# Kernel tuning notes

Measured on AMD Instinct MI355X. Metric: run time of the kernel, lower is better.

## Reference

```python
import jax, jax.numpy as jnp
import numpy as np

# ---- config (mirrors init_kwargs) ----
D_MODEL = 1024
D_STATE = 128
EXPAND = 2
HEADDIM = 64
D_INNER = D_MODEL * EXPAND            # 2048
NHEADS = D_INNER // HEADDIM           # 32
ROPE_FRACTION = 0.5
ROTATE_DIM = (int(D_STATE * ROPE_FRACTION) // 2) * 2   # 64
NUM_ANGLES = ROTATE_DIM // 2          # 32
A_FLOOR = 1e-4
EPS = 1e-5
IN_PROJ_DIM = 2 * D_INNER + 2 * D_STATE + 3 * NHEADS + NUM_ANGLES  # 4480
BATCH, SEQLEN = 2, 2048


def _state_rmsnorm(x, w):
    rms = jnp.sqrt(jnp.mean(x * x, axis=-1, keepdims=True) + EPS)
    return x / rms * w


def _apply_rotary_pairs(x, phase):
    # x: (b,s,h,d_state), phase: (b,s,h,num_pairs)
    if ROTATE_DIM == 0:
        return x
    x_rot = x[..., :ROTATE_DIM].reshape(*x.shape[:-1], ROTATE_DIM // 2, 2)
    x_pass = x[..., ROTATE_DIM:]
    cos = jnp.cos(phase)
    sin = jnp.sin(phase)
    real = x_rot[..., 0]
    imag = x_rot[..., 1]
    rr = real * cos - imag * sin
    ri = real * sin + imag * cos
    rotated = jnp.stack([rr, ri], axis=-1).reshape(*x.shape[:-1], ROTATE_DIM)
    if x_pass.shape[-1] == 0:
        return rotated
    return jnp.concatenate([rotated, x_pass], axis=-1)


def setup_inputs() -> dict:
    key = jax.random.key(0)
    ks = jax.random.split(key, 5)
    x = jax.random.normal(ks[0], (BATCH, SEQLEN, D_MODEL), jnp.float32)
    W_in = jax.random.normal(ks[1], (IN_PROJ_DIM, D_MODEL), jnp.float32) / np.sqrt(D_MODEL)
    # dt_bias ~ inverse-softplus of dt sampled in [dt_min, dt_max]
    dt = jnp.exp(jax.random.uniform(ks[2], (NHEADS,), jnp.float32) * (np.log(0.1) - np.log(0.001)) + np.log(0.001))
    dt = jnp.clip(dt, 1e-4)
    dt_bias = dt + jnp.log(-jnp.expm1(-dt))
    B_norm_w = jnp.ones((D_STATE,), jnp.float32)
    C_norm_w = jnp.ones((D_STATE,), jnp.float32)
    B_bias = jnp.ones((NHEADS, D_STATE), jnp.float32)
    C_bias = jnp.ones((NHEADS, D_STATE), jnp.float32)
    D_param = jnp.ones((NHEADS,), jnp.float32)
    out_norm_w = jnp.ones((D_INNER,), jnp.float32)
    W_out = jax.random.normal(ks[3], (D_MODEL, D_INNER), jnp.float32) / np.sqrt(D_INNER)
    return {"x": x, "W_in": W_in, "dt_bias": dt_bias, "B_norm_w": B_norm_w,
            "C_norm_w": C_norm_w, "B_bias": B_bias, "C_bias": C_bias,
            "D_param": D_param, "out_norm_w": out_norm_w, "W_out": W_out}


def reference(x, W_in, dt_bias, B_norm_w, C_norm_w, B_bias, C_bias, D_param, out_norm_w, W_out):
    b, s, _ = x.shape
    proj = jnp.einsum('bsd,pd->bsp', x, W_in)
    sizes = [D_INNER, D_INNER, D_STATE, D_STATE, NHEADS, NHEADS, NHEADS, NUM_ANGLES]
    offs = np.cumsum([0] + sizes)
    z, v, B_raw, C_raw, dd_dt, dd_A, trap_logits, angle_logits = [
        proj[..., offs[i]:offs[i + 1]] for i in range(8)]
    z = z.reshape(b, s, NHEADS, HEADDIM)
    v = v.reshape(b, s, NHEADS, HEADDIM)
    Bm = _state_rmsnorm(B_raw, B_norm_w)[:, :, None, :] + B_bias[None, None]   # (b,s,h,n)
    Cm = _state_rmsnorm(C_raw, C_norm_w)[:, :, None, :] + C_bias[None, None]
    dt = jax.nn.softplus(dd_dt + dt_bias[None, None])          # (b,s,h)
    A = jnp.minimum(-jax.nn.softplus(dd_A), -A_FLOOR)          # (b,s,h)
    trap = jax.nn.sigmoid(trap_logits)                          # (b,s,h)
    phase = jnp.cumsum(angle_logits, axis=1)[:, :, None, :]     # (b,s,1,angles)
    phase = jnp.broadcast_to(phase, (b, s, NHEADS, NUM_ANGLES))
    Bm = _apply_rotary_pairs(Bm, phase)
    Cm = _apply_rotary_pairs(Cm, phase)

    alpha = jnp.exp(A * dt)               # (b,s,h)
    beta = (1.0 - trap) * dt * alpha
    gamma = trap * dt

    # move time to leading for scan: (s, b, h, ...)
    def tl(a):
        return jnp.moveaxis(a, 1, 0)
    xs = (tl(alpha), tl(beta), tl(gamma), tl(Bm), tl(Cm), tl(v))

    state0 = jnp.zeros((b, NHEADS, HEADDIM, D_STATE), jnp.float32)
    pk0 = jnp.zeros((b, NHEADS, D_STATE), jnp.float32)
    pv0 = jnp.zeros((b, NHEADS, HEADDIM), jnp.float32)

    def step(carry, inp):
        state, pk, pv = carry
        a_t, b_t, g_t, k_t, q_t, v_t = inp
        prev_outer = pv[..., :, None] * pk[..., None, :]        # (b,h,p,n)
        curr_outer = v_t[..., :, None] * k_t[..., None, :]
        state = (a_t[..., None, None] * state
                 + b_t[..., None, None] * prev_outer
                 + g_t[..., None, None] * curr_outer)
        y_t = jnp.einsum('bhpn,bhn->bhp', state, q_t) + D_param[None, :, None] * v_t
        return (state, k_t, v_t), y_t

    _, ys = jax.lax.scan(step, (state0, pk0, pv0), xs)
    y = jnp.moveaxis(ys, 0, 1).reshape(b, s, D_INNER)
    z = z.reshape(b, s, D_INNER)
    # GatedRMSNorm
    rms = jnp.sqrt(jnp.mean(y * y, axis=-1, keepdims=True) + EPS)
    y = (y / rms * out_norm_w) * jax.nn.silu(z)
    return jnp.einsum('bsi,di->bsd', y, W_out)
```

## Files before the change

### kernel.cpp

```cpp
#include <hip/hip_runtime.h>
#include <math.h>

#define S_LEN 2048
#define NBATCH 2
#define DMODEL 1024
#define PDIM 4480
#define DI 2048
#define NH 32
#define HD 64
#define DS 128
#define NA 32
#define CHK 64
#define NC (S_LEN / CHK)
#define ZV 4096
#define PS 384
#define PS_B 0
#define PS_C 128
#define PS_DT 256
#define PS_A 288
#define PS_TRAP 320
#define PS_ANG 352

typedef __attribute__((ext_vector_type(8))) short s8v;
typedef __attribute__((ext_vector_type(4))) float f4v;

__device__ __forceinline__ float softplus_f(float x) {
    return x > 20.f ? x : log1pf(expf(x));
}

__device__ __forceinline__ ushort f2bf(float f) {
    unsigned u = __float_as_uint(f);
    unsigned r = (u + 0x7fffu + ((u >> 16) & 1u)) >> 16;
    return (ushort)r;
}

__device__ __forceinline__ uint4 pack8(const float* f) {
    uint4 o;
    o.x = (unsigned)f2bf(f[0]) | ((unsigned)f2bf(f[1]) << 16);
    o.y = (unsigned)f2bf(f[2]) | ((unsigned)f2bf(f[3]) << 16);
    o.z = (unsigned)f2bf(f[4]) | ((unsigned)f2bf(f[5]) << 16);
    o.w = (unsigned)f2bf(f[6]) | ((unsigned)f2bf(f[7]) << 16);
    return o;
}

__device__ __forceinline__ float bf2f(ushort u) {
    return __uint_as_float(((unsigned)u) << 16);
}
__device__ __forceinline__ float bf_lo(unsigned u) { return __uint_as_float(u << 16); }
__device__ __forceinline__ float bf_hi(unsigned u) { return __uint_as_float(u & 0xffff0000u); }

__device__ __forceinline__ void unpack8(uint4 a, float* f) {
    f[0] = bf_lo(a.x); f[1] = bf_hi(a.x);
    f[2] = bf_lo(a.y); f[3] = bf_hi(a.y);
    f[4] = bf_lo(a.z); f[5] = bf_hi(a.z);
    f[6] = bf_lo(a.w); f[7] = bf_hi(a.w);
}

#define NCX  524288
#define NCWI 573440
#define NCWO 262144
__global__ __launch_bounds__(256)
void f2bf_all(const float* __restrict__ x, const float* __restrict__ wi,
              const float* __restrict__ wo, ushort* __restrict__ xbf,
              ushort* __restrict__ wibf, ushort* __restrict__ wobf) {
    int idx = blockIdx.x * 256 + threadIdx.x;
    const float* src; ushort* dst; int shift, rel;
    if (idx < NCX)              { rel = idx;               src = x;  dst = xbf;  shift = 7; }
    else if (idx < NCX + NCWI)  { rel = idx - NCX;         src = wi; dst = wibf; shift = 7; }
    else                        { rel = idx - NCX - NCWI;  src = wo; dst = wobf; shift = 8; }
    int dc = rel ^ ((rel >> shift) & 7);
    const float* ip = src + (size_t)rel * 8;
    float4 v0 = *(const float4*)ip;
    float4 v1 = *(const float4*)(ip + 4);
    uint4 o;
    o.x = (unsigned)f2bf(v0.x) | ((unsigned)f2bf(v0.y) << 16);
    o.y = (unsigned)f2bf(v0.z) | ((unsigned)f2bf(v0.w) << 16);
    o.z = (unsigned)f2bf(v1.x) | ((unsigned)f2bf(v1.y) << 16);
    o.w = (unsigned)f2bf(v1.z) | ((unsigned)f2bf(v1.w) << 16);
    *(uint4*)(dst + (size_t)dc * 8) = o;
}

__global__ __launch_bounds__(256, 2)
void gemm_bf16(const ushort* __restrict__ A, const ushort* __restrict__ B,
               float* __restrict__ Cf, ushort* __restrict__ Cb,
               int M, int N, int K, int split, int fstride, int SW) {
    __shared__ __align__(16) short lAB[2][128 * 64];
    short* lA = &lAB[0][0];
    short* lB = &lAB[1][0];
    int nwg = gridDim.x;
    int bid = blockIdx.x;
    int chunk = nwg >> 3;
    int swz = (bid & 7) * chunk + (bid >> 3);
    int nb = N >> 7;
    int sup = 4 * SW;
    int st = swz / sup, w = swz % sup;
    int stPerRow = nb / SW;
    int by = (st / stPerRow) * 4 + w / SW;
    int bx = (st % stPerRow) * SW + w % SW;

    int tid = threadIdx.x;
    int wv = tid >> 6, ln = tid & 63;
    int rl = ln & 15, kg = ln >> 4, r7 = rl & 7;
    int R0 = (wv >> 1) * 64, C0 = (wv & 1) * 64;

    const ushort* Ag = A + (size_t)(by * 128 + wv * 32 + (ln >> 3)) * K + (ln & 7) * 8;
    const ushort* Bg = B + (size_t)(bx * 128 + wv * 32 + (ln >> 3)) * K + (ln & 7) * 8;
    short* lAw = lA + (wv * 32) * 64;
    short* lBw = lB + (wv * 32) * 64;

    f4v acc[4][4];
#pragma unroll
    for (int m = 0; m < 4; ++m)
#pragma unroll
        for (int n = 0; n < 4; ++n) acc[m][n] = f4v{0.f, 0.f, 0.f, 0.f};

    for (int k0 = 0; k0 < K; k0 += 64) {
        __syncthreads();
#pragma unroll
        for (int i = 0; i < 4; ++i) {
            __builtin_amdgcn_global_load_lds(
                (const __attribute__((address_space(1))) void*)(Ag + (size_t)i * 8 * K + k0),
                (__attribute__((address_space(3))) void*)(lAw + i * 8 * 64), 16, 0, 0);
            __builtin_amdgcn_global_load_lds(
                (const __attribute__((address_space(1))) void*)(Bg + (size_t)i * 8 * K + k0),
                (__attribute__((address_space(3))) void*)(lBw + i * 8 * 64), 16, 0, 0);
        }
        __syncthreads();
#pragma unroll
        for (int ks = 0; ks < 2; ++ks) {
            int kc = ks * 4 + kg;
            int co = ((kc ^ r7) << 3);
            s8v av[4], bv[4];
#pragma unroll
            for (int m = 0; m < 4; ++m)
                av[m] = *(const s8v*)&lA[(R0 + m * 16 + rl) * 64 + co];
#pragma unroll
            for (int n = 0; n < 4; ++n)
                bv[n] = *(const s8v*)&lB[(C0 + n * 16 + rl) * 64 + co];
#pragma unroll
            for (int m = 0; m < 4; ++m)
#pragma unroll
                for (int n = 0; n < 4; ++n)
                    acc[m][n] = __builtin_amdgcn_mfma_f32_16x16x32_bf16(
                        av[m], bv[n], acc[m][n], 0, 0, 0);
        }
    }
    if (bx * 128 < split) {
        __syncthreads();
        ushort* ct = (ushort*)lAB;
#pragma unroll
        for (int m = 0; m < 4; ++m)
#pragma unroll
            for (int n = 0; n < 4; ++n)
#pragma unroll
                for (int r = 0; r < 4; ++r)
                    ct[(R0 + m * 16 + kg * 4 + r) * 128 + C0 + n * 16 + rl] =
                        f2bf(acc[m][n][r]);
        __syncthreads();
        ushort* cb = Cb + (size_t)(by * 128) * split + bx * 128;
        const uint4* cs = (const uint4*)ct;
#pragma unroll
        for (int k = 0; k < 8; ++k) {
            int idx = k * 256 + tid;
            int row = idx >> 4, cc = idx & 15;
            *(uint4*)(cb + (size_t)row * split + cc * 8) = cs[idx];
        }
    } else {
#pragma unroll
        for (int hp = 0; hp < 2; ++hp) {
            __syncthreads();
            float* cf = (float*)lAB;
            if ((wv & 1) == hp) {
#pragma unroll
                for (int m = 0; m < 4; ++m)
#pragma unroll
                    for (int n = 0; n < 4; ++n)
#pragma unroll
                        for (int r = 0; r < 4; ++r)
                            cf[(R0 + m * 16 + kg * 4 + r) * 64 + n * 16 + rl] =
                                acc[m][n][r];
            }
            __syncthreads();
            float* co = Cf + (size_t)(by * 128) * fstride + (bx * 128 - split) + hp * 64;
            const float4* fs = (const float4*)cf;
#pragma unroll
            for (int k = 0; k < 8; ++k) {
                int idx = k * 256 + tid;
                int row = idx >> 4, c4 = idx & 15;
                *(float4*)(co + (size_t)row * fstride + c4 * 4) = fs[idx];
            }
        }
    }
}

__global__ __launch_bounds__(256)
void phase_kernel(const float* __restrict__ projS, float* __restrict__ cosb,
                  float* __restrict__ sinb) {
    int b = blockIdx.x >> 5;
    int j = blockIdx.x & 31;
    int tid = threadIdx.x;
    __shared__ float part[256];
    float v[8];
    float run = 0.f;
#pragma unroll
    for (int e = 0; e < 8; ++e) {
        int s = tid * 8 + e;
        v[e] = projS[((size_t)(b * S_LEN + s)) * PS + PS_ANG + j];
        run += v[e];
    }
    part[tid] = run;
    __syncthreads();
    for (int off = 1; off < 256; off <<= 1) {
        float add = (tid >= off) ? part[tid - off] : 0.f;
        __syncthreads();
        part[tid] += add;
        __syncthreads();
    }
    float acc = (tid > 0) ? part[tid - 1] : 0.f;
#pragma unroll
    for (int e = 0; e < 8; ++e) {
        acc += v[e];
        int s = tid * 8 + e;
        size_t o = ((size_t)(b * S_LEN + s)) * NA + j;
        cosb[o] = cosf(acc);
        sinb[o] = sinf(acc);
    }
}

__global__ __launch_bounds__(128)
void prep_kernel(const float* __restrict__ projS, const float* __restrict__ dt_bias,
                 const float* __restrict__ Bw, const float* __restrict__ Cw,
                 const float* __restrict__ cosb, const float* __restrict__ sinb,
                 float* __restrict__ Bn, float* __restrict__ Cn,
                 float* __restrict__ ldb, float* __restrict__ wbuf,
                 float* __restrict__ pubuf) {
    size_t row = blockIdx.x;
    int b = (int)(row >> 11);
    int s = (int)(row & 2047);
    int n = threadIdx.x;
    const float* pr = projS + row * PS;
    float vB = pr[PS_B + n];
    float vC = pr[PS_C + n];
    float sB = vB * vB, sC = vC * vC;
#pragma unroll
    for (int off = 32; off >= 1; off >>= 1) {
        sB += __shfl_xor(sB, off);
        sC += __shfl_xor(sC, off);
    }
    __shared__ float redB[2], redC[2];
    if ((n & 63) == 0) { redB[n >> 6] = sB; redC[n >> 6] = sC; }
    __syncthreads();
    float rB = sqrtf((redB[0] + redB[1]) * (1.f / 128.f) + 1e-5f);
    float rC = sqrtf((redC[0] + redC[1]) * (1.f / 128.f) + 1e-5f);
    float bn = vB / rB * Bw[n];
    float cn = vC / rC * Cw[n];
    float bp = __shfl_xor(bn, 1);
    float cp = __shfl_xor(cn, 1);
    float ob = bn, oc = cn;
    if (n < 64) {
        float c = cosb[row * NA + (n >> 1)];
        float sn_ = sinb[row * NA + (n >> 1)];
        if ((n & 1) == 0) { ob = bn * c - bp * sn_; oc = cn * c - cp * sn_; }
        else              { ob = bp * sn_ + bn * c; oc = cp * sn_ + cn * c; }
    }
    Bn[row * DS + n] = ob;
    Cn[row * DS + n] = oc;
    if (n < NH) {
        int h = n;
        float dtv = softplus_f(pr[PS_DT + h] + dt_bias[h]);
        float Av = -fmaxf(softplus_f(pr[PS_A + h]), 1e-4f);
        float trap = 1.f / (1.f + expf(-pr[PS_TRAP + h]));
        size_t o = ((size_t)(b * NH + h)) * S_LEN + s;
        ldb[o]   = Av * dtv;
        wbuf[o]  = trap * dtv;
        pubuf[o] = (1.f - trap) * dtv;
    }
}

__global__ __launch_bounds__(256)
void lcum_kernel(float* __restrict__ ell) {
    size_t row = blockIdx.x;
    int tid = threadIdx.x;
    float* p = ell + row * S_LEN;
    float v[8];
    float run = 0.f;
#pragma unroll
    for (int e = 0; e < 8; ++e) { v[e] = p[tid * 8 + e]; run += v[e]; }
    __shared__ float part[256];
    part[tid] = run;
    __syncthreads();
    for (int off = 1; off < 256; off <<= 1) {
        float add = (tid >= off) ? part[tid - off] : 0.f;
        __syncthreads();
        part[tid] += add;
        __syncthreads();
    }
    float acc = (tid > 0) ? part[tid - 1] : 0.f;
#pragma unroll
    for (int e = 0; e < 8; ++e) { acc += v[e]; p[tid * 8 + e] = acc; }
}

__device__ __forceinline__ void build32v(
    float* vals, const float* __restrict__ br, const float* __restrict__ bias,
    const float* __restrict__ cr, const float* __restrict__ sr, int rot) {
    float bv[32], bi[32];
#pragma unroll
    for (int j = 0; j < 8; ++j) *(float4*)&bv[j * 4] = *(const float4*)(br + j * 4);
#pragma unroll
    for (int j = 0; j < 8; ++j) *(float4*)&bi[j * 4] = *(const float4*)(bias + j * 4);
    if (rot) {
        float cf[16], sf[16];
#pragma unroll
        for (int j = 0; j < 4; ++j) {
            *(float4*)&cf[j * 4] = *(const float4*)(cr + j * 4);
            *(float4*)&sf[j * 4] = *(const float4*)(sr + j * 4);
        }
#pragma unroll
        for (int a = 0; a < 16; ++a) {
            float c = cf[a], s = sf[a], e = bi[2 * a], o = bi[2 * a + 1];
            vals[2 * a]     = bv[2 * a]     + e * c - o * s;
            vals[2 * a + 1] = bv[2 * a + 1] + e * s + o * c;
        }
    } else {
#pragma unroll
        for (int j = 0; j < 32; ++j) vals[j] = bv[j] + bi[j];
    }
}

__global__ __launch_bounds__(256, 4)
void delta_kernel(const ushort* __restrict__ zvbf, const float* __restrict__ Bn,
                  const float* __restrict__ cosb, const float* __restrict__ sinb,
                  const float* __restrict__ ell, const float* __restrict__ wbuf,
                  const float* __restrict__ pubuf, const float* __restrict__ B_bias,
                  ushort* __restrict__ dstate, ushort* __restrict__ vtbuf,
                  ushort* __restrict__ kbuf, float* __restrict__ rbuf) {
    __shared__ __align__(16) ushort KT[DS * CHK];
    __shared__ __align__(16) ushort cVT[HD * CHK];
    __shared__ __align__(16) ushort VT[HD * CHK];
    int blk = blockIdx.x;
    int c = blk & (NC - 1);
    int h = (blk >> 5) & (NH - 1);
    int b = blk >> 10;
    int tid = threadIdx.x;
    size_t row0 = (size_t)b * S_LEN + c * CHK;
    size_t bh = (size_t)b * NH + h;
    int i = tid >> 2, q4 = tid & 3;

    size_t so = bh * S_LEN + c * CHK + i;
    float llast = ell[bh * S_LEN + c * CHK + CHK - 1];
    float li = ell[so];
    float u = wbuf[so];
    if (c * CHK + i < S_LEN - 1) u += pubuf[so + 1];
    float coef = expf(llast - li) * u;
    if (tid == 0) {
        float base = (c == 0) ? 0.f : ell[bh * S_LEN + c * CHK - 1];
        rbuf[blk] = expf(llast - base);
    }
    {
        int n0 = q4 * 32;
        float vals[32];
        build32v(vals, Bn + (row0 + i) * DS + n0, B_bias + h * DS + n0,
                 cosb + (row0 + i) * NA + q4 * 16, sinb + (row0 + i) * NA + q4 * 16,
                 q4 < 2);
#pragma unroll
        for (int j = 0; j < 32; ++j) {
            int n = n0 + j;
            KT[n * 64 + (((i >> 3) ^ (n & 7)) << 3) + (i & 7)] = f2bf(vals[j]);
        }
        ushort* kd = kbuf + (size_t)blk * (CHK * DS);
#pragma unroll
        for (int j = 0; j < 4; ++j) {
            int cc = (q4 * 4 + j) ^ (i & 7);
            *(uint4*)&kd[i * 128 + cc * 8] = pack8(&vals[j * 8]);
        }
    }
    {
        int p0 = q4 * 16;
        const ushort* vp = zvbf + (size_t)(row0 + i) * ZV + 2048 + h * HD + p0;
        uint4 a0 = *(const uint4*)vp;
        uint4 a1 = *(const uint4*)(vp + 8);
        unsigned uu[8] = {a0.x, a0.y, a0.z, a0.w, a1.x, a1.y, a1.z, a1.w};
#pragma unroll
        for (int j = 0; j < 8; ++j) {
            ushort v0 = (ushort)(uu[j] & 0xffffu);
            ushort v1 = (ushort)(uu[j] >> 16);
            int p = p0 + 2 * j;
            int addr0 = p * 64 + (((i >> 3) ^ (p & 7)) << 3) + (i & 7);
            int addr1 = (p + 1) * 64 + (((i >> 3) ^ ((p + 1) & 7)) << 3) + (i & 7);
            VT[addr0]  = v0;
            VT[addr1]  = v1;
            cVT[addr0] = f2bf(bf2f(v0) * coef);
            cVT[addr1] = f2bf(bf2f(v1) * coef);
        }
    }
    __syncthreads();
    {
        const uint4* vs = (const uint4*)VT;
        uint4* vd = (uint4*)(vtbuf + (size_t)blk * (HD * CHK));
        vd[tid] = vs[tid];
        vd[tid + 256] = vs[tid + 256];
    }
    int wv = tid >> 6, ln = tid & 63, rl = ln & 15, kg = ln >> 4;
    int pA = wv * 16 + rl;
    s8v aV[2];
#pragma unroll
    for (int ks = 0; ks < 2; ++ks)
        aV[ks] = *(const s8v*)&cVT[pA * 64 + (((ks * 4 + kg) ^ (pA & 7)) << 3)];
    f4v dacc[8];
    __builtin_amdgcn_s_setprio(1);
#pragma unroll
    for (int nt = 0; nt < 8; ++nt) {
        int nB = nt * 16 + rl;
        dacc[nt] = f4v{0.f, 0.f, 0.f, 0.f};
#pragma unroll
        for (int ks = 0; ks < 2; ++ks) {
            s8v bK = *(const s8v*)&KT[nB * 64 + (((ks * 4 + kg) ^ (nB & 7)) << 3)];
            dacc[nt] = __builtin_amdgcn_mfma_f32_16x16x32_bf16(aV[ks], bK, dacc[nt], 0, 0, 0);
        }
    }
    __builtin_amdgcn_s_setprio(0);
    __syncthreads();
#pragma unroll
    for (int nt = 0; nt < 8; ++nt) {
#pragma unroll
        for (int r = 0; r < 4; ++r) {
            int p = wv * 16 + kg * 4 + r;
            int n = nt * 16 + rl;
            KT[p * 128 + (((n >> 3) ^ (p & 7)) << 3) + (n & 7)] = f2bf(dacc[nt][r]);
        }
    }
    __syncthreads();
    {
        const uint4* dsr = (const uint4*)KT;
        uint4* dd = (uint4*)(dstate + (size_t)blk * (HD * DS));
#pragma unroll
        for (int k = 0; k < 4; ++k) dd[k * 256 + tid] = dsr[k * 256 + tid];
    }
}

__global__ __launch_bounds__(256)
void state_prop(ushort* __restrict__ dstate, const float* __restrict__ rbuf) {
    int g = blockIdx.x;
    size_t bh = (size_t)(g >> 2);
    int sl = g & 3;
    int tid = threadIdx.x;
    float st[8];
#pragma unroll
    for (int j = 0; j < 8; ++j) st[j] = 0.f;
    uint4* base = (uint4*)dstate;
    size_t off0 = bh * NC * 1024ull + (size_t)sl * 256 + tid;
    uint4 nxt = base[off0];
    for (int c = 0; c < NC; ++c) {
        uint4 cur = nxt;
        if (c + 1 < NC) nxt = base[off0 + (size_t)(c + 1) * 1024];
        float r = rbuf[bh * NC + c];
        unsigned uu[4] = {cur.x, cur.y, cur.z, cur.w};
        unsigned oo[4];
#pragma unroll
        for (int e = 0; e < 4; ++e) {
            float d0 = bf_lo(uu[e]), d1 = bf_hi(uu[e]);
            int ix = e * 2;
            oo[e] = (unsigned)f2bf(st[ix]) | ((unsigned)f2bf(st[ix + 1]) << 16);
            st[ix]     = fmaf(r, st[ix], d0);
            st[ix + 1] = fmaf(r, st[ix + 1], d1);
        }
        base[off0 + (size_t)c * 1024] = uint4{oo[0], oo[1], oo[2], oo[3]};
    }
}

__global__ __launch_bounds__(256, 4)
void out_kernel(const float* __restrict__ Cn, const float* __restrict__ cosb,
                const float* __restrict__ sinb, const float* __restrict__ ell,
                const float* __restrict__ wbuf, const float* __restrict__ pubuf,
                const float* __restrict__ C_bias, const ushort* __restrict__ dstate,
                const ushort* __restrict__ vtbuf, const ushort* __restrict__ kbuf,
                float* __restrict__ yb) {
    __shared__ __align__(16) ushort Qb[CHK * DS];
    __shared__ __align__(16) ushort Kb[CHK * DS];
    __shared__ __align__(16) ushort VTb[HD * CHK];
    int blk = blockIdx.x;
    int c = blk & (NC - 1);
    int h = (blk >> 5) & (NH - 1);
    int b = blk >> 10;
    int tid = threadIdx.x;
    size_t row0 = (size_t)b * S_LEN + c * CHK;
    size_t bh = (size_t)b * NH + h;
    int i = tid >> 2, q4 = tid & 3;
    int wv2 = tid >> 6, ln = tid & 63;

    {
        const ushort* kg_ = kbuf + (size_t)blk * (CHK * DS);
#pragma unroll
        for (int k = 0; k < 4; ++k) {
            int ch = wv2 * 256 + k * 64;
            __builtin_amdgcn_global_load_lds(
                (const __attribute__((address_space(1))) void*)(kg_ + (size_t)(ch + ln) * 8),
                (__attribute__((address_space(3))) void*)(Kb + ch * 8), 16, 0, 0);
        }
        const ushort* vg = vtbuf + (size_t)blk * (HD * CHK);
#pragma unroll
        for (int k = 0; k < 2; ++k) {
            int ch = wv2 * 128 + k * 64;
            __builtin_amdgcn_global_load_lds(
                (const __attribute__((address_space(1))) void*)(vg + (size_t)(ch + ln) * 8),
                (__attribute__((address_space(3))) void*)(VTb + ch * 8), 16, 0, 0);
        }
    }
    {
        int n0 = q4 * 32;
        float vals[32];
        build32v(vals, Cn + (row0 + i) * DS + n0, C_bias + h * DS + n0,
                 cosb + (row0 + i) * NA + q4 * 16, sinb + (row0 + i) * NA + q4 * 16,
                 q4 < 2);
#pragma unroll
        for (int j = 0; j < 4; ++j) {
            int cc = (q4 * 4 + j) ^ (i & 7);
            *(uint4*)&Qb[i * 128 + cc * 8] = pack8(&vals[j * 8]);
        }
    }
    __syncthreads();

    int rl = ln & 15, kg = ln >> 4;
    int tA = wv2 * 16 + rl;
    s8v aQ[4];
#pragma unroll
    for (int kc = 0; kc < 4; ++kc)
        aQ[kc] = *(const s8v*)&Qb[tA * 128 + (((kc * 4 + kg) ^ (tA & 7)) << 3)];
    f4v pacc[4];
#pragma unroll
    for (int st = 0; st < 4; ++st) pacc[st] = f4v{0.f, 0.f, 0.f, 0.f};
    __builtin_amdgcn_s_setprio(1);
#pragma unroll
    for (int st = 0; st < 4; ++st) {
        int sB = st * 16 + rl;
#pragma unroll
        for (int kc = 0; kc < 4; ++kc) {
            s8v bK = *(const s8v*)&Kb[sB * 128 + (((kc * 4 + kg) ^ (sB & 7)) << 3)];
            pacc[st] = __builtin_amdgcn_mfma_f32_16x16x32_bf16(aQ[kc], bK, pacc[st], 0, 0, 0);
        }
    }
    __builtin_amdgcn_s_setprio(0);
    __syncthreads();

    {
        const ushort* sg = dstate + (size_t)blk * (CHK * DS);
#pragma unroll
        for (int k = 0; k < 4; ++k) {
            int ch = wv2 * 256 + k * 64;
            __builtin_amdgcn_global_load_lds(
                (const __attribute__((address_space(1))) void*)(sg + (size_t)(ch + ln) * 8),
                (__attribute__((address_space(3))) void*)(Kb + ch * 8), 16, 0, 0);
        }
    }
    size_t so0 = bh * S_LEN + c * CHK;
    float basev = (c == 0) ? 0.f : ell[so0 - 1];
    int t2r0 = wv2 * 16 + kg * 4;
    float et[4], wr[4];
#pragma unroll
    for (int r = 0; r < 4; ++r) {
        size_t so = so0 + t2r0 + r;
        et[r] = expf(ell[so] - basev);
        wr[r] = wbuf[so];
    }
    float fs[4];
#pragma unroll
    for (int st = 0; st < 4; ++st) {
        int s = st * 16 + rl;
        size_t sos = so0 + s;
        float u = wbuf[sos];
        if (c * CHK + s < S_LEN - 1) u += pubuf[sos + 1];
        fs[st] = u * expf(fminf(basev - ell[sos], 80.f));
    }
    ushort* PTb = Qb;
#pragma unroll
    for (int st = 0; st < 4; ++st) {
        int s = st * 16 + rl;
#pragma unroll
        for (int r = 0; r < 4; ++r) {
            int t2 = t2r0 + r;
            float m;
            if (s < t2)       m = et[r] * fs[st];
            else if (s == t2) m = wr[r];
            else              m = 0.f;
            PTb[t2 * 64 + (((s >> 3) ^ (t2 & 7)) << 3) + (s & 7)] = f2bf(pacc[st][r] * m);
        }
    }
    __syncthreads();

    s8v aP[2];
#pragma unroll
    for (int ks = 0; ks < 2; ++ks)
        aP[ks] = *(const s8v*)&PTb[tA * 64 + (((ks * 4 + kg) ^ (tA & 7)) << 3)];
    f4v y1[4], y2[4];
#pragma unroll
    for (int pt = 0; pt < 4; ++pt) { y1[pt] = f4v{0.f,0.f,0.f,0.f}; y2[pt] = f4v{0.f,0.f,0.f,0.f}; }
    __builtin_amdgcn_s_setprio(1);
#pragma unroll
    for (int pt = 0; pt < 4; ++pt) {
        int pB = pt * 16 + rl;
#pragma unroll
        for (int ks = 0; ks < 2; ++ks) {
            s8v bV = *(const s8v*)&VTb[pB * 64 + (((ks * 4 + kg) ^ (pB & 7)) << 3)];
            y1[pt] = __builtin_amdgcn_mfma_f32_16x16x32_bf16(aP[ks], bV, y1[pt], 0, 0, 0);
        }
#pragma unroll
        for (int kc = 0; kc < 4; ++kc) {
            s8v bS = *(const s8v*)&Kb[pB * 128 + (((kc * 4 + kg) ^ (pB & 7)) << 3)];
            y2[pt] = __builtin_amdgcn_mfma_f32_16x16x32_bf16(aQ[kc], bS, y2[pt], 0, 0, 0);
        }
    }
    __builtin_amdgcn_s_setprio(0);
    __syncthreads();
    float* ct = (float*)Qb;
#pragma unroll
    for (int pt = 0; pt < 4; ++pt) {
#pragma unroll
        for (int r = 0; r < 4; ++r) {
            int t2 = t2r0 + r;
            int p = pt * 16 + rl;
            ct[t2 * 64 + p] = y1[pt][r] + et[r] * y2[pt][r];
        }
    }
    __syncthreads();
    {
        float* yp = yb + (size_t)blk * (CHK * HD);
        const float4* fsrc = (const float4*)ct;
#pragma unroll
        for (int k = 0; k < 4; ++k) {
            int idx = k * 256 + tid;
            *(float4*)(yp + idx * 4) = fsrc[idx];
        }
    }
}

__global__ __launch_bounds__(256)
void ynorm_kernel(const float* __restrict__ yb, const ushort* __restrict__ zvbf,
                  const float* __restrict__ w, const float* __restrict__ D_param,
                  ushort* __restrict__ ybf) {
    size_t row = blockIdx.x;
    int b = (int)(row >> 11);
    int s = (int)(row & 2047);
    int c = s >> 6, t = s & 63;
    int tid = threadIdx.x;
    int hh = tid >> 3;
    int p0 = (tid * 8) & 63;
    const float* yr = yb + (((size_t)(b * NH + hh) * NC + c) * CHK + t) * HD + p0;
    float4 v0 = *(const float4*)yr;
    float4 v1 = *(const float4*)(yr + 4);
    float vvf[8];
    unpack8(*(const uint4*)(zvbf + row * (size_t)ZV + 2048 + tid * 8), vvf);
    float Dp = D_param[hh];
    float yv[8] = {v0.x + Dp * vvf[0], v0.y + Dp * vvf[1], v0.z + Dp * vvf[2], v0.w + Dp * vvf[3],
                   v1.x + Dp * vvf[4], v1.y + Dp * vvf[5], v1.z + Dp * vvf[6], v1.w + Dp * vvf[7]};
    float ss = 0.f;
#pragma unroll
    for (int e = 0; e < 8; ++e) ss += yv[e] * yv[e];
#pragma unroll
    for (int off = 32; off >= 1; off >>= 1) ss += __shfl_xor(ss, off);
    __shared__ float red[4];
    if ((tid & 63) == 0) red[tid >> 6] = ss;
    __syncthreads();
    float tot = red[0] + red[1] + red[2] + red[3];
    float rinv = 1.f / sqrtf(tot * (1.f / 2048.f) + 1e-5f);
    float zv[8];
    unpack8(*(const uint4*)(zvbf + row * (size_t)ZV + tid * 8), zv);
    float4 w0 = *(const float4*)(w + tid * 8);
    float4 w1 = *(const float4*)(w + tid * 8 + 4);
    float wv[8] = {w0.x, w0.y, w0.z, w0.w, w1.x, w1.y, w1.z, w1.w};
    ushort u[8];
#pragma unroll
    for (int e = 0; e < 8; ++e) {
        float sil = zv[e] / (1.f + expf(-zv[e]));
        u[e] = f2bf(yv[e] * rinv * wv[e] * sil);
    }
    int dstc = (tid & ~7) | ((tid & 7) ^ ((int)row & 7));
    uint4 o;
    o.x = (unsigned)u[0] | ((unsigned)u[1] << 16);
    o.y = (unsigned)u[2] | ((unsigned)u[3] << 16);
    o.z = (unsigned)u[4] | ((unsigned)u[5] << 16);
    o.w = (unsigned)u[6] | ((unsigned)u[7] << 16);
    *(uint4*)(ybf + row * (size_t)DI + dstc * 8) = o;
}

extern "C" void kernel_launch(void* const* d_in, const int* in_sizes, int n_in,
                              void* d_out, int out_size, void* d_ws, size_t ws_size,
                              hipStream_t stream) {
    const float* x          = (const float*)d_in[0];
    const float* W_in       = (const float*)d_in[1];
    const float* dt_bias    = (const float*)d_in[2];
    const float* B_norm_w   = (const float*)d_in[3];
    const float* C_norm_w   = (const float*)d_in[4];
    const float* B_bias     = (const float*)d_in[5];
    const float* C_bias     = (const float*)d_in[6];
    const float* D_param    = (const float*)d_in[7];
    const float* out_norm_w = (const float*)d_in[8];
    const float* W_out      = (const float*)d_in[9];
    float* out = (float*)d_out;

    const size_t M = (size_t)NBATCH * S_LEN;
    const size_t NBLK = (size_t)NBATCH * NH * NC;
    float* ws = (float*)d_ws;
    size_t off = 0;
    float* projS = ws + off; off += M * PS;
    float* cosb  = ws + off; off += M * NA;
    float* sinb  = ws + off; off += M * NA;
    float* Bn    = ws + off; off += M * DS;
    float* Cn    = ws + off; off += M * DS;
    float* ell   = ws + off; off += (size_t)NBATCH * NH * S_LEN;
    float* wbuf  = ws + off; off += (size_t)NBATCH * NH * S_LEN;
    float* pubuf = ws + off; off += (size_t)NBATCH * NH * S_LEN;
    float* yb    = ws + off; off += NBLK * CHK * HD;
    float* rbuf  = ws + off; off += NBLK;
    ushort* zvbf = (ushort*)(ws + off); off += M * ZV / 2;
    ushort* xbf  = (ushort*)(ws + off); off += M * DMODEL / 2;
    ushort* wibf = (ushort*)(ws + off); off += (size_t)PDIM * DMODEL / 2;
    ushort* wobf = (ushort*)(ws + off); off += (size_t)DMODEL * DI / 2;
    ushort* ybf  = (ushort*)(ws + off); off += M * DI / 2;
    ushort* dstate = (ushort*)(ws + off); off += NBLK * CHK * DS / 2;
    ushort* vtbuf  = (ushort*)(ws + off); off += NBLK * HD * CHK / 2;
    ushort* kbuf   = (ushort*)(ws + off); off += NBLK * CHK * DS / 2;

    f2bf_all<<<dim3((NCX + NCWI + NCWO) / 256), 256, 0, stream>>>(
        x, W_in, W_out, xbf, wibf, wobf);
    gemm_bf16<<<dim3((PDIM / 128) * (int)(M / 128)), 256, 0, stream>>>(
        xbf, wibf, projS, zvbf, (int)M, PDIM, DMODEL, ZV, PS, 5);
    phase_kernel<<<dim3(NBATCH * NA), 256, 0, stream>>>(projS, cosb, sinb);
    prep_kernel<<<dim3((int)M), 128, 0, stream>>>(projS, dt_bias, B_norm_w, C_norm_w,
                                                  cosb, sinb, Bn, Cn, ell, wbuf, pubuf);
    lcum_kernel<<<dim3(NBATCH * NH), 256, 0, stream>>>(ell);
    delta_kernel<<<dim3((int)NBLK), 256, 0, stream>>>(zvbf, Bn, cosb, sinb, ell,
                                                      wbuf, pubuf, B_bias, dstate,
                                                      vtbuf, kbuf, rbuf);
    state_prop<<<dim3(NBATCH * NH * 4), 256, 0, stream>>>(dstate, rbuf);
    out_kernel<<<dim3((int)NBLK), 256, 0, stream>>>(Cn, cosb, sinb, ell,
                                                    wbuf, pubuf, C_bias,
                                                    dstate, vtbuf, kbuf, yb);
    ynorm_kernel<<<dim3((int)M), 256, 0, stream>>>(yb, zvbf, out_norm_w, D_param, ybf);
    gemm_bf16<<<dim3((DMODEL / 128) * (int)(M / 128)), 256, 0, stream>>>(
        ybf, wobf, out, nullptr, (int)M, DMODEL, DI, 0, DMODEL, 4);
}
```

Measured before the change: 216.4 us.

## Move intra-chunk output into delta kernel; leave only inter-chunk term for post-scan

```diff
diff --git a/kernel.cpp b/kernel.cpp
--- a/kernel.cpp
+++ b/kernel.cpp
@@ -327,15 +327,17 @@
     }
 }
 
-__global__ __launch_bounds__(256, 4)
-void delta_kernel(const ushort* __restrict__ zvbf, const float* __restrict__ Bn,
-                  const float* __restrict__ cosb, const float* __restrict__ sinb,
-                  const float* __restrict__ ell, const float* __restrict__ wbuf,
-                  const float* __restrict__ pubuf, const float* __restrict__ B_bias,
-                  ushort* __restrict__ dstate, ushort* __restrict__ vtbuf,
-                  ushort* __restrict__ kbuf, float* __restrict__ rbuf) {
-    __shared__ __align__(16) ushort KT[DS * CHK];
-    __shared__ __align__(16) ushort cVT[HD * CHK];
+__global__ __launch_bounds__(256, 2)
+void intra_kernel(const ushort* __restrict__ zvbf, const float* __restrict__ Bn,
+                  const float* __restrict__ Cn, const float* __restrict__ cosb,
+                  const float* __restrict__ sinb, const float* __restrict__ ell,
+                  const float* __restrict__ wbuf, const float* __restrict__ pubuf,
+                  const float* __restrict__ B_bias, const float* __restrict__ C_bias,
+                  ushort* __restrict__ dstate, ushort* __restrict__ qbuf,
+                  float* __restrict__ yb, float* __restrict__ rbuf) {
+    __shared__ __align__(16) ushort cKT[DS * CHK];
+    __shared__ __align__(16) ushort bufK[CHK * DS];
+    __shared__ __align__(16) ushort bufQ[CHK * DS];
     __shared__ __align__(16) ushort VT[HD * CHK];
     int blk = blockIdx.x;
     int c = blk & (NC - 1);
@@ -363,15 +365,26 @@
                  cosb + (row0 + i) * NA + q4 * 16, sinb + (row0 + i) * NA + q4 * 16,
                  q4 < 2);
 #pragma unroll
+        for (int j = 0; j < 4; ++j) {
+            int cc = (q4 * 4 + j) ^ (i & 7);
+            *(uint4*)&bufK[i * 128 + cc * 8] = pack8(&vals[j * 8]);
+        }
+#pragma unroll
         for (int j = 0; j < 32; ++j) {
             int n = n0 + j;
-            KT[n * 64 + (((i >> 3) ^ (n & 7)) << 3) + (i & 7)] = f2bf(vals[j]);
-        }
-        ushort* kd = kbuf + (size_t)blk * (CHK * DS);
+            cKT[n * 64 + (((i >> 3) ^ (n & 7)) << 3) + (i & 7)] = f2bf(vals[j] * coef);
+        }
+    }
+    {
+        int n0 = q4 * 32;
+        float vals[32];
+        build32v(vals, Cn + (row0 + i) * DS + n0, C_bias + h * DS + n0,
+                 cosb + (row0 + i) * NA + q4 * 16, sinb + (row0 + i) * NA + q4 * 16,
+                 q4 < 2);
 #pragma unroll
         for (int j = 0; j < 4; ++j) {
             int cc = (q4 * 4 + j) ^ (i & 7);
-            *(uint4*)&kd[i * 128 + cc * 8] = pack8(&vals[j * 8]);
+            *(uint4*)&bufQ[i * 128 + cc * 8] = pack8(&vals[j * 8]);
         }
     }
     {
@@ -385,56 +398,143 @@
             ushort v0 = (ushort)(uu[j] & 0xffffu);
             ushort v1 = (ushort)(uu[j] >> 16);
             int p = p0 + 2 * j;
-            int addr0 = p * 64 + (((i >> 3) ^ (p & 7)) << 3) + (i & 7);
-            int addr1 = (p + 1) * 64 + (((i >> 3) ^ ((p + 1) & 7)) << 3) + (i & 7);
-            VT[addr0]  = v0;
-            VT[addr1]  = v1;
-            cVT[addr0] = f2bf(bf2f(v0) * coef);
-            cVT[addr1] = f2bf(bf2f(v1) * coef);
-        }
-    }
-    __syncthreads();
-    {
-        const uint4* vs = (const uint4*)VT;
-        uint4* vd = (uint4*)(vtbuf + (size_t)blk * (HD * CHK));
-        vd[tid] = vs[tid];
-        vd[tid + 256] = vs[tid + 256];
-    }
-    int wv = tid >> 6, ln = tid & 63, rl = ln & 15, kg = ln >> 4;
-    int pA = wv * 16 + rl;
+            VT[p * 64 + (((i >> 3) ^ (p & 7)) << 3) + (i & 7)] = v0;
+            VT[(p + 1) * 64 + (((i >> 3) ^ ((p + 1) & 7)) << 3) + (i & 7)] = v1;
+        }
+    }
+    __syncthreads();
+
+    int wv2 = tid >> 6, ln = tid & 63, rl = ln & 15, kg = ln >> 4;
+    int tA = wv2 * 16 + rl;
+    s8v aQ[4];
+#pragma unroll
+    for (int kc = 0; kc < 4; ++kc)
+        aQ[kc] = *(const s8v*)&bufQ[tA * 128 + (((kc * 4 + kg) ^ (tA & 7)) << 3)];
     s8v aV[2];
 #pragma unroll
     for (int ks = 0; ks < 2; ++ks)
-        aV[ks] = *(const s8v*)&cVT[pA * 64 + (((ks * 4 + kg) ^ (pA & 7)) << 3)];
+        aV[ks] = *(const s8v*)&VT[tA * 64 + (((ks * 4 + kg) ^ (tA & 7)) << 3)];
+    f4v pacc[4];
+#pragma unroll
+    for (int st = 0; st < 4; ++st) pacc[st] = f4v{0.f, 0.f, 0.f, 0.f};
     f4v dacc[8];
+#pragma unroll
+    for (int nt = 0; nt < 8; ++nt) dacc[nt] = f4v{0.f, 0.f, 0.f, 0.f};
     __builtin_amdgcn_s_setprio(1);
+#pragma unroll
+    for (int st = 0; st < 4; ++st) {
+        int sB = st * 16 + rl;
+#pragma unroll
+        for (int kc = 0; kc < 4; ++kc) {
+            s8v bK = *(const s8v*)&bufK[sB * 128 + (((kc * 4 + kg) ^ (sB & 7)) << 3)];
+            pacc[st] = __builtin_amdgcn_mfma_f32_16x16x32_bf16(aQ[kc], bK, pacc[st], 0, 0, 0);
+        }
+    }
 #pragma unroll
     for (int nt = 0; nt < 8; ++nt) {
         int nB = nt * 16 + rl;
-        dacc[nt] = f4v{0.f, 0.f, 0.f, 0.f};
 #pragma unroll
         for (int ks = 0; ks < 2; ++ks) {
-            s8v bK = *(const s8v*)&KT[nB * 64 + (((ks * 4 + kg) ^ (nB & 7)) << 3)];
+            s8v bK = *(const s8v*)&cKT[nB * 64 + (((ks * 4 + kg) ^ (nB & 7)) << 3)];
             dacc[nt] = __builtin_amdgcn_mfma_f32_16x16x32_bf16(aV[ks], bK, dacc[nt], 0, 0, 0);
         }
     }
     __builtin_amdgcn_s_setprio(0);
-    __syncthreads();
+    {
+        const uint4* qs = (const uint4*)bufQ;
+        uint4* qd = (uint4*)(qbuf + (size_t)blk * (CHK * DS));
+#pragma unroll
+        for (int k = 0; k < 4; ++k) qd[k * 256 + tid] = qs[k * 256 + tid];
+    }
+    __syncthreads();
+
+    size_t so0 = bh * S_LEN + c * CHK;
+    float basev = (c == 0) ? 0.f : ell[so0 - 1];
+    int t2r0 = wv2 * 16 + kg * 4;
+    float et[4], wr[4];
+#pragma unroll
+    for (int r = 0; r < 4; ++r) {
+        size_t sor = so0 + t2r0 + r;
+        et[r] = expf(ell[sor] - basev);
+        wr[r] = wbuf[sor];
+    }
+    float fs[4];
+#pragma unroll
+    for (int st = 0; st < 4; ++st) {
+        int s = st * 16 + rl;
+        size_t sos = so0 + s;
+        float uu = wbuf[sos];
+        if (c * CHK + s < S_LEN - 1) uu += pubuf[sos + 1];
+        fs[st] = uu * expf(fminf(basev - ell[sos], 80.f));
+    }
+    ushort* PTb = bufK;
+#pragma unroll
+    for (int st = 0; st < 4; ++st) {
+        int s = st * 16 + rl;
+#pragma unroll
+        for (int r = 0; r < 4; ++r) {
+            int t2 = t2r0 + r;
+            float m;
+            if (s < t2)       m = et[r] * fs[st];
+            else if (s == t2) m = wr[r];
+            else              m = 0.f;
+            PTb[t2 * 64 + (((s >> 3) ^ (t2 & 7)) << 3) + (s & 7)] = f2bf(pacc[st][r] * m);
+        }
+    }
 #pragma unroll
     for (int nt = 0; nt < 8; ++nt) {
 #pragma unroll
         for (int r = 0; r < 4; ++r) {
-            int p = wv * 16 + kg * 4 + r;
+            int p = wv2 * 16 + kg * 4 + r;
             int n = nt * 16 + rl;
-            KT[p * 128 + (((n >> 3) ^ (p & 7)) << 3) + (n & 7)] = f2bf(dacc[nt][r]);
-        }
-    }
-    __syncthreads();
+            cKT[p * 128 + (((n >> 3) ^ (p & 7)) << 3) + (n & 7)] = f2bf(dacc[nt][r]);
+        }
+    }
+    __syncthreads();
+
     {
-        const uint4* dsr = (const uint4*)KT;
+        const uint4* dsr = (const uint4*)cKT;
         uint4* dd = (uint4*)(dstate + (size_t)blk * (HD * DS));
 #pragma unroll
         for (int k = 0; k < 4; ++k) dd[k * 256 + tid] = dsr[k * 256 + tid];
+    }
+    s8v aP[2];
+#pragma unroll
+    for (int ks = 0; ks < 2; ++ks)
+        aP[ks] = *(const s8v*)&PTb[tA * 64 + (((ks * 4 + kg) ^ (tA & 7)) << 3)];
+    f4v y1[4];
+#pragma unroll
+    for (int pt = 0; pt < 4; ++pt) y1[pt] = f4v{0.f, 0.f, 0.f, 0.f};
+    __builtin_amdgcn_s_setprio(1);
+#pragma unroll
+    for (int pt = 0; pt < 4; ++pt) {
+        int pB = pt * 16 + rl;
+#pragma unroll
+        for (int ks = 0; ks < 2; ++ks) {
+            s8v bV = *(const s8v*)&VT[pB * 64 + (((ks * 4 + kg) ^ (pB & 7)) << 3)];
+            y1[pt] = __builtin_amdgcn_mfma_f32_16x16x32_bf16(aP[ks], bV, y1[pt], 0, 0, 0);
+        }
+    }
+    __builtin_amdgcn_s_setprio(0);
+    float* ct = (float*)bufQ;
+#pragma unroll
+    for (int pt = 0; pt < 4; ++pt) {
+#pragma unroll
+        for (int r = 0; r < 4; ++r) {
+            int t2 = t2r0 + r;
+            int p = pt * 16 + rl;
+            ct[t2 * 64 + p] = y1[pt][r];
+        }
+    }
+    __syncthreads();
+    {
+        float* yp = yb + (size_t)blk * (CHK * HD);
+        const float4* fsrc = (const float4*)ct;
+#pragma unroll
+        for (int k = 0; k < 4; ++k) {
+            int idx = k * 256 + tid;
+            *(float4*)(yp + idx * 4) = fsrc[idx];
+        }
     }
 }
 
@@ -469,144 +569,57 @@
 }
 
 __global__ __launch_bounds__(256, 4)
-void out_kernel(const float* __restrict__ Cn, const float* __restrict__ cosb,
-                const float* __restrict__ sinb, const float* __restrict__ ell,
-                const float* __restrict__ wbuf, const float* __restrict__ pubuf,
-                const float* __restrict__ C_bias, const ushort* __restrict__ dstate,
-                const ushort* __restrict__ vtbuf, const ushort* __restrict__ kbuf,
-                float* __restrict__ yb) {
+void y2_kernel(const ushort* __restrict__ qbuf, const ushort* __restrict__ dstate,
+               const float* __restrict__ ell, float* __restrict__ yb) {
     __shared__ __align__(16) ushort Qb[CHK * DS];
-    __shared__ __align__(16) ushort Kb[CHK * DS];
-    __shared__ __align__(16) ushort VTb[HD * CHK];
+    __shared__ __align__(16) ushort Sb[CHK * DS];
     int blk = blockIdx.x;
     int c = blk & (NC - 1);
     int h = (blk >> 5) & (NH - 1);
     int b = blk >> 10;
     int tid = threadIdx.x;
-    size_t row0 = (size_t)b * S_LEN + c * CHK;
     size_t bh = (size_t)b * NH + h;
-    int i = tid >> 2, q4 = tid & 3;
     int wv2 = tid >> 6, ln = tid & 63;
 
     {
-        const ushort* kg_ = kbuf + (size_t)blk * (CHK * DS);
+        const ushort* qg = qbuf + (size_t)blk * (CHK * DS);
+        const ushort* sg = dstate + (size_t)blk * (CHK * DS);
 #pragma unroll
         for (int k = 0; k < 4; ++k) {
             int ch = wv2 * 256 + k * 64;
             __builtin_amdgcn_global_load_lds(
-                (const __attribute__((address_space(1))) void*)(kg_ + (size_t)(ch + ln) * 8),
-                (__attribute__((address_space(3))) void*)(Kb + ch * 8), 16, 0, 0);
-        }
-        const ushort* vg = vtbuf + (size_t)blk * (HD * CHK);
-#pragma unroll
-        for (int k = 0; k < 2; ++k) {
-            int ch = wv2 * 128 + k * 64;
+                (const __attribute__((address_space(1))) void*)(qg + (size_t)(ch + ln) * 8),
+                (__attribute__((address_space(3))) void*)(Qb + ch * 8), 16, 0, 0);
             __builtin_amdgcn_global_load_lds(
-                (const __attribute__((address_space(1))) void*)(vg + (size_t)(ch + ln) * 8),
-                (__attribute__((address_space(3))) void*)(VTb + ch * 8), 16, 0, 0);
-        }
-    }
-    {
-        int n0 = q4 * 32;
-        float vals[32];
-        build32v(vals, Cn + (row0 + i) * DS + n0, C_bias + h * DS + n0,
-                 cosb + (row0 + i) * NA + q4 * 16, sinb + (row0 + i) * NA + q4 * 16,
-                 q4 < 2);
-#pragma unroll
-        for (int j = 0; j < 4; ++j) {
-            int cc = (q4 * 4 + j) ^ (i & 7);
-            *(uint4*)&Qb[i * 128 + cc * 8] = pack8(&vals[j * 8]);
-        }
-    }
-    __syncthreads();
-
+                (const __attribute__((address_space(1))) void*)(sg + (size_t)(ch + ln) * 8),
+                (__attribute__((address_space(3))) void*)(Sb + ch * 8), 16, 0, 0);
+        }
+    }
+    size_t so0 = bh * S_LEN + c * CHK;
+    float basev = (c == 0) ? 0.f : ell[so0 - 1];
     int rl = ln & 15, kg = ln >> 4;
+    int t2r0 = wv2 * 16 + kg * 4;
+    float et[4];
+#pragma unroll
+    for (int r = 0; r < 4; ++r) et[r] = expf(ell[so0 + t2r0 + r] - basev);
+    __syncthreads();
+
     int tA = wv2 * 16 + rl;
     s8v aQ[4];
 #pragma unroll
     for (int kc = 0; kc < 4; ++kc)
         aQ[kc] = *(const s8v*)&Qb[tA * 128 + (((kc * 4 + kg) ^ (tA & 7)) << 3)];
-    f4v pacc[4];
-#pragma unroll
-    for (int st = 0; st < 4; ++st) pacc[st] = f4v{0.f, 0.f, 0.f, 0.f};
-    __builtin_amdgcn_s_setprio(1);
-#pragma unroll
-    for (int st = 0; st < 4; ++st) {
-        int sB = st * 16 + rl;
-#pragma unroll
-        for (int kc = 0; kc < 4; ++kc) {
-            s8v bK = *(const s8v*)&Kb[sB * 128 + (((kc * 4 + kg) ^ (sB & 7)) << 3)];
-            pacc[st] = __builtin_amdgcn_mfma_f32_16x16x32_bf16(aQ[kc], bK, pacc[st], 0, 0, 0);
-        }
-    }
-    __builtin_amdgcn_s_setprio(0);
-    __syncthreads();
-
-    {
-        const ushort* sg = dstate + (size_t)blk * (CHK * DS);
-#pragma unroll
-        for (int k = 0; k < 4; ++k) {
-            int ch = wv2 * 256 + k * 64;
-            __builtin_amdgcn_global_load_lds(
-                (const __attribute__((address_space(1))) void*)(sg + (size_t)(ch + ln) * 8),
-                (__attribute__((address_space(3))) void*)(Kb + ch * 8), 16, 0, 0);
-        }
-    }
-    size_t so0 = bh * S_LEN + c * CHK;
-    float basev = (c == 0) ? 0.f : ell[so0 - 1];
-    int t2r0 = wv2 * 16 + kg * 4;
-    float et[4], wr[4];
-#pragma unroll
-    for (int r = 0; r < 4; ++r) {
-        size_t so = so0 + t2r0 + r;
-        et[r] = expf(ell[so] - basev);
-        wr[r] = wbuf[so];
-    }
-    float fs[4];
-#pragma unroll
-    for (int st = 0; st < 4; ++st) {
-        int s = st * 16 + rl;
-        size_t sos = so0 + s;
-        float u = wbuf[sos];
-        if (c * CHK + s < S_LEN - 1) u += pubuf[sos + 1];
-        fs[st] = u * expf(fminf(basev - ell[sos], 80.f));
-    }
-    ushort* PTb = Qb;
-#pragma unroll
-    for (int st = 0; st < 4; ++st) {
-        int s = st * 16 + rl;
-#pragma unroll
-        for (int r = 0; r < 4; ++r) {
-            int t2 = t2r0 + r;
-            float m;
-            if (s < t2)       m = et[r] * fs[st];
-            else if (s == t2) m = wr[r];
-            else              m = 0.f;
-            PTb[t2 * 64 + (((s >> 3) ^ (t2 & 7)) << 3) + (s & 7)] = f2bf(pacc[st][r] * m);
-        }
-    }
-    __syncthreads();
-
-    s8v aP[2];
-#pragma unroll
-    for (int ks = 0; ks < 2; ++ks)
-        aP[ks] = *(const s8v*)&PTb[tA * 64 + (((ks * 4 + kg) ^ (tA & 7)) << 3)];
-    f4v y1[4], y2[4];
-#pragma unroll
-    for (int pt = 0; pt < 4; ++pt) { y1[pt] = f4v{0.f,0.f,0.f,0.f}; y2[pt] = f4v{0.f,0.f,0.f,0.f}; }
+    f4v y2a[4];
+#pragma unroll
+    for (int pt = 0; pt < 4; ++pt) y2a[pt] = f4v{0.f, 0.f, 0.f, 0.f};
     __builtin_amdgcn_s_setprio(1);
 #pragma unroll
     for (int pt = 0; pt < 4; ++pt) {
         int pB = pt * 16 + rl;
 #pragma unroll
-        for (int ks = 0; ks < 2; ++ks) {
-            s8v bV = *(const s8v*)&VTb[pB * 64 + (((ks * 4 + kg) ^ (pB & 7)) << 3)];
-            y1[pt] = __builtin_amdgcn_mfma_f32_16x16x32_bf16(aP[ks], bV, y1[pt], 0, 0, 0);
-        }
-#pragma unroll
         for (int kc = 0; kc < 4; ++kc) {
-            s8v bS = *(const s8v*)&Kb[pB * 128 + (((kc * 4 + kg) ^ (pB & 7)) << 3)];
-            y2[pt] = __builtin_amdgcn_mfma_f32_16x16x32_bf16(aQ[kc], bS, y2[pt], 0, 0, 0);
+            s8v bS = *(const s8v*)&Sb[pB * 128 + (((kc * 4 + kg) ^ (pB & 7)) << 3)];
+            y2a[pt] = __builtin_amdgcn_mfma_f32_16x16x32_bf16(aQ[kc], bS, y2a[pt], 0, 0, 0);
         }
     }
     __builtin_amdgcn_s_setprio(0);
@@ -618,7 +631,7 @@
         for (int r = 0; r < 4; ++r) {
             int t2 = t2r0 + r;
             int p = pt * 16 + rl;
-            ct[t2 * 64 + p] = y1[pt][r] + et[r] * y2[pt][r];
+            ct[t2 * 64 + p] = et[r] * y2a[pt][r];
         }
     }
     __syncthreads();
@@ -628,7 +641,10 @@
 #pragma unroll
         for (int k = 0; k < 4; ++k) {
             int idx = k * 256 + tid;
-            *(float4*)(yp + idx * 4) = fsrc[idx];
+            float4 cur = *(const float4*)(yp + idx * 4);
+            float4 add = fsrc[idx];
+            cur.x += add.x; cur.y += add.y; cur.z += add.z; cur.w += add.w;
+            *(float4*)(yp + idx * 4) = cur;
         }
     }
 }
@@ -717,8 +733,7 @@
     ushort* wobf = (ushort*)(ws + off); off += (size_t)DMODEL * DI / 2;
     ushort* ybf  = (ushort*)(ws + off); off += M * DI / 2;
     ushort* dstate = (ushort*)(ws + off); off += NBLK * CHK * DS / 2;
-    ushort* vtbuf  = (ushort*)(ws + off); off += NBLK * HD * CHK / 2;
-    ushort* kbuf   = (ushort*)(ws + off); off += NBLK * CHK * DS / 2;
+    ushort* qbuf   = (ushort*)(ws + off); off += NBLK * CHK * DS / 2;
 
     f2bf_all<<<dim3((NCX + NCWI + NCWO) / 256), 256, 0, stream>>>(
         x, W_in, W_out, xbf, wibf, wobf);
@@ -728,13 +743,11 @@
     prep_kernel<<<dim3((int)M), 128, 0, stream>>>(projS, dt_bias, B_norm_w, C_norm_w,
                                                   cosb, sinb, Bn, Cn, ell, wbuf, pubuf);
     lcum_kernel<<<dim3(NBATCH * NH), 256, 0, stream>>>(ell);
-    delta_kernel<<<dim3((int)NBLK), 256, 0, stream>>>(zvbf, Bn, cosb, sinb, ell,
-                                                      wbuf, pubuf, B_bias, dstate,
-                                                      vtbuf, kbuf, rbuf);
+    intra_kernel<<<dim3((int)NBLK), 256, 0, stream>>>(zvbf, Bn, Cn, cosb, sinb, ell,
+                                                      wbuf, pubuf, B_bias, C_bias,
+                                                      dstate, qbuf, yb, rbuf);
     state_prop<<<dim3(NBATCH * NH * 4), 256, 0, stream>>>(dstate, rbuf);
-    out_kernel<<<dim3((int)NBLK), 256, 0, stream>>>(Cn, cosb, sinb, ell,
-                                                    wbuf, pubuf, C_bias,
-                                                    dstate, vtbuf, kbuf, yb);
+    y2_kernel<<<dim3((int)NBLK), 256, 0, stream>>>(qbuf, dstate, ell, yb);
     ynorm_kernel<<<dim3((int)M), 256, 0, stream>>>(yb, zvbf, out_norm_w, D_param, ybf);
     gemm_bf16<<<dim3((DMODEL / 128) * (int)(M / 128)), 256, 0, stream>>>(
         ybf, wobf, out, nullptr, (int)M, DMODEL, DI, 0, DMODEL, 4);
```

Measured after the change: 225.1 us. +4.0%, slower.
